# Kernel tuning notes

Hardware: AMD Instinct MI355X
Metric: run time of the kernel (lower is better)

Reference implementation:

```python
import jax, jax.numpy as jnp
import numpy as np

B, C, N, S, DCONV = 16, 128, 2000, 8, 4
DI = 2 * N            # mamba expand=2
DT_RANK = (N + 15) // 16


def setup_inputs() -> dict:
    key = jax.random.key(0)
    ks = jax.random.split(key, 10)
    r = lambda k, sh, s=0.02: jax.random.normal(k, sh, jnp.float32) * s
    return {
        "x": jax.random.normal(ks[0], (B, C, N, 1), jnp.float32),
        "bn1_g": jnp.ones((C,), jnp.float32), "bn1_b": jnp.zeros((C,), jnp.float32),
        "conv1_w": r(ks[1], (C, C)), "conv1_b": jnp.zeros((C,), jnp.float32),
        "ln_w": jnp.ones((N,), jnp.float32), "ln_b": jnp.zeros((N,), jnp.float32),
        "W_in": r(ks[2], (2 * DI, N)),
        "convm_w": r(ks[3], (DI, DCONV), 0.1), "convm_b": jnp.zeros((DI,), jnp.float32),
        "W_x": r(ks[4], (DT_RANK + 2 * S, DI)),
        "W_dt": r(ks[5], (DI, DT_RANK), 0.1), "b_dt": jnp.full((DI,), -2.0, jnp.float32),
        "A_log": jnp.log(jnp.broadcast_to(jnp.arange(1, S + 1, dtype=jnp.float32), (DI, S))),
        "D_p": jnp.ones((DI,), jnp.float32),
        "W_out": r(ks[6], (N, DI)),
        "bn3_g": jnp.ones((C,), jnp.float32), "bn3_b": jnp.zeros((C,), jnp.float32),
        "conv3_w": r(ks[7], (C, C)), "conv3_b": jnp.zeros((C,), jnp.float32),
    }


def _inorm(x, eps=1e-3):
    # InstanceNorm2d (no affine): per-sample, per-channel over spatial dims
    m = x.mean(axis=(2, 3), keepdims=True)
    v = x.var(axis=(2, 3), keepdims=True)
    return (x - m) * jax.lax.rsqrt(v + eps)


def _bnorm(x, g, b, eps=1e-5):
    # BatchNorm2d (training-mode stats) over (B, H, W) per channel
    m = x.mean(axis=(0, 2, 3), keepdims=True)
    v = x.var(axis=(0, 2, 3), keepdims=True)
    return (x - m) * jax.lax.rsqrt(v + eps) * g[None, :, None, None] + b[None, :, None, None]


def _block(x, g, b, w, cb):
    # InstanceNorm -> BatchNorm -> ReLU -> 1x1 Conv2d
    h = jax.nn.relu(_bnorm(_inorm(x), g, b))
    return jnp.einsum('bcnw,oc->bonw', h, w) + cb[None, :, None, None]


def _mamba(u, W_in, cw, cb, W_x, W_dt, b_dt, A_log, D_p, W_out):
    # u: [B, L, D] with L=C (seq), D=N (d_model)
    L = u.shape[1]
    xz = jnp.einsum('bld,ed->ble', u, W_in)          # [B,L,2*DI]
    xi, z = jnp.split(xz, 2, axis=-1)
    # depthwise causal conv1d along L (d_conv=4)
    xp = jnp.pad(xi, ((0, 0), (DCONV - 1, 0), (0, 0)))
    xc = sum(xp[:, k:k + L, :] * cw[:, k] for k in range(DCONV)) + cb
    xc = jax.nn.silu(xc)                             # [B,L,DI]
    xdbl = jnp.einsum('bld,ed->ble', xc, W_x)        # [B,L,dt_rank+2S]
    dt = jax.nn.softplus(jnp.einsum('blr,dr->bld', xdbl[..., :DT_RANK], W_dt) + b_dt)
    Bm = xdbl[..., DT_RANK:DT_RANK + S]              # [B,L,S]
    Cm = xdbl[..., DT_RANK + S:]                     # [B,L,S]
    A = -jnp.exp(A_log)                              # [DI,S]

    def step(h, inp):
        dt_l, B_l, C_l, u_l = inp                    # [B,DI],[B,S],[B,S],[B,DI]
        dA = jnp.exp(dt_l[..., None] * A)            # [B,DI,S]
        h = dA * h + (dt_l * u_l)[..., None] * B_l[:, None, :]
        return h, jnp.einsum('bds,bs->bd', h, C_l)

    seq = (jnp.swapaxes(dt, 0, 1), jnp.swapaxes(Bm, 0, 1),
           jnp.swapaxes(Cm, 0, 1), jnp.swapaxes(xc, 0, 1))
    h0 = jnp.zeros((u.shape[0], DI, S), u.dtype)
    _, ys = jax.lax.scan(step, h0, seq)              # ys: [L,B,DI]
    y = jnp.swapaxes(ys, 0, 1) + xc * D_p
    y = y * jax.nn.silu(z)
    return jnp.einsum('ble,de->bld', y, W_out)       # [B,L,D]


def reference(x, bn1_g, bn1_b, conv1_w, conv1_b, ln_w, ln_b, W_in, convm_w,
              convm_b, W_x, W_dt, b_dt, A_log, D_p, W_out, bn3_g, bn3_b,
              conv3_w, conv3_b):
    out = _block(x, bn1_g, bn1_b, conv1_w, conv1_b)[..., 0]   # [B,C,N]
    mu = out.mean(-1, keepdims=True)
    var = out.var(-1, keepdims=True)
    out_n = (out - mu) * jax.lax.rsqrt(var + 1e-5) * ln_w + ln_b  # LayerNorm(points)
    out = out + _mamba(out_n, W_in, convm_w, convm_b, W_x, W_dt, b_dt, A_log, D_p, W_out)
    out = _block(out[..., None], bn3_g, bn3_b, conv3_w, conv3_b)  # [B,C,N,1]
    return out + x
```

## Files before the change

### kernel.cpp

```cpp
#include <hip/hip_runtime.h>
#include <cmath>
#include <cstdint>

#define Bc   16
#define Cc   128
#define Nc   2000
#define Lc   128
#define DIc  4000
#define Sc   8
#define RKc  125
#define E2c  8000
#define EXc  141

#define KP1  2048
#define NP8  8192
#define KT8  32

__device__ __forceinline__ unsigned short f2bf(float f) {
  union { float f; unsigned int u; } v; v.f = f;
  unsigned int r = v.u + 0x7FFFu + ((v.u >> 16) & 1u);
  return (unsigned short)(r >> 16);
}

__global__ void inorm_stats(const float* __restrict__ in,
                            float* __restrict__ mout,
                            float* __restrict__ vout) {
  int bc = blockIdx.x;
  const float* p = in + (long)bc * Nc;
  float s = 0.f, sq = 0.f;
  for (int i = threadIdx.x; i < Nc; i += blockDim.x) {
    float x = p[i]; s += x; sq += x * x;
  }
  #pragma unroll
  for (int o = 32; o > 0; o >>= 1) {
    s  += __shfl_down(s, o, 64);
    sq += __shfl_down(sq, o, 64);
  }
  __shared__ float ss[4], sqq[4];
  int w = threadIdx.x >> 6, lane = threadIdx.x & 63;
  if (lane == 0) { ss[w] = s; sqq[w] = sq; }
  __syncthreads();
  if (threadIdx.x == 0) {
    s  = ss[0] + ss[1] + ss[2] + ss[3];
    sq = sqq[0] + sqq[1] + sqq[2] + sqq[3];
    float mean = s / Nc;
    float var  = sq / Nc - mean * mean;
    mout[bc] = mean; vout[bc] = var;
  }
}

__global__ void compute_h_t(const float* __restrict__ in,
                            const float* __restrict__ m,
                            const float* __restrict__ v,
                            const float* __restrict__ g,
                            const float* __restrict__ bb,
                            unsigned short* __restrict__ hT) {
  int b  = blockIdx.y;
  int n0 = blockIdx.x * 64;
  __shared__ unsigned short tile[64][132];
  __shared__ float bnsc_s[128];
  int t  = threadIdx.x;
  if (t < 128) {
    float s = 0.f;
    #pragma unroll
    for (int bb2 = 0; bb2 < Bc; bb2++) {
      float vv = v[bb2 * Cc + t];
      s += vv / (vv + 1e-3f);
    }
    bnsc_s[t] = rsqrtf(s / Bc + 1e-5f);
  }
  __syncthreads();
  int nl = t & 63, cb = t >> 6;
  int n  = n0 + nl;
  #pragma unroll 4
  for (int p = 0; p < 32; p++) {
    int c = p * 4 + cb;
    float val = 0.f;
    if (n < Nc) {
      int bc = b * Cc + c;
      float xn = (in[(long)bc * Nc + n] - m[bc]) * rsqrtf(v[bc] + 1e-3f);
      val = fmaxf(xn * bnsc_s[c] * g[c] + bb[c], 0.f);
    }
    tile[nl][c] = f2bf(val);
  }
  __syncthreads();
  int r = t >> 2, c0 = (t & 3) * 32;
  int nr = n0 + r;
  if (nr < Nc) {
    unsigned int* dst = (unsigned int*)(hT + ((long)b * 2048 + nr) * 128 + c0);
    const unsigned short* src = &tile[r][c0];
    #pragma unroll
    for (int j = 0; j < 16; j++)
      dst[j] = *(const unsigned int*)(src + 2 * j);
  }
}

__global__ void reduce_slices(const float* __restrict__ sl, float* __restrict__ dst,
                              long stride, int ns, int total, int accum) {
  int i = blockIdx.x * 256 + threadIdx.x;
  if (i >= total) return;
  float s = accum ? dst[i] : 0.f;
  for (int k = 0; k < ns; k++) s += sl[(long)k * stride + i];
  dst[i] = s;
}

__global__ void reduce_xdbl(const float* __restrict__ sl,
                            float* __restrict__ xd,
                            unsigned short* __restrict__ xdb) {
  int i = blockIdx.x * 256 + threadIdx.x;
  if (i >= 2048 * 144) return;
  int row = i / 144, c = i - row * 144;
  float s = 0.f;
  if (c < EXc) {
    #pragma unroll
    for (int k = 0; k < 4; k++) s += sl[(long)k * (2048 * 256) + (long)row * 256 + c];
    xd[(long)row * EXc + c] = s;
  }
  if (c < 128) xdb[(long)row * 128 + c] = f2bf(c < RKc ? s : 0.f);
}

__global__ void cvt_pad_bf16(const float* __restrict__ src, unsigned short* __restrict__ dst,
                             int R, int Cdst, int Rsrc, int Csrc) {
  long i = (long)blockIdx.x * 256 + threadIdx.x;
  long total = (long)R * Cdst;
  if (i >= total) return;
  int r = (int)(i / Cdst), c = (int)(i - (long)r * Cdst);
  float v = (r < Rsrc && c < Csrc) ? src[(long)r * Csrc + c] : 0.f;
  dst[i] = f2bf(v);
}

__global__ void cvt_convw2(const float* __restrict__ w1, const float* __restrict__ w3,
                           unsigned short* __restrict__ d1, unsigned short* __restrict__ d3) {
  int i = blockIdx.x * 256 + threadIdx.x;
  if (i < 16384) d1[i] = f2bf(w1[i]);
  else if (i < 32768) d3[i - 16384] = f2bf(w3[i - 16384]);
}

__global__ void cvt_wx_wdt(const float* __restrict__ Wx, const float* __restrict__ Wdt,
                           unsigned short* __restrict__ bwx, unsigned short* __restrict__ bwdt) {
  int i = blockIdx.x * 256 + threadIdx.x;
  if (i < 256 * 4000) {
    int r = i / 4000, c = i - r * 4000;
    bwx[i] = f2bf(r < EXc ? Wx[(long)r * 4000 + c] : 0.f);
  } else {
    int j = i - 256 * 4000;
    if (j < 4096 * 128) {
      int r = j >> 7, c = j & 127;
      bwdt[j] = f2bf((r < DIc && c < RKc) ? Wdt[(long)r * RKc + c] : 0.f);
    }
  }
}

__global__ void ln_rows(const float* __restrict__ in,
                        const float* __restrict__ lw,
                        const float* __restrict__ lb,
                        unsigned short* __restrict__ An) {
  int row = blockIdx.x;
  const float* p = in + (long)row * Nc;
  float s = 0.f, sq = 0.f;
  for (int i = threadIdx.x; i < Nc; i += blockDim.x) {
    float x = p[i]; s += x; sq += x * x;
  }
  #pragma unroll
  for (int o = 32; o > 0; o >>= 1) {
    s  += __shfl_down(s, o, 64);
    sq += __shfl_down(sq, o, 64);
  }
  __shared__ float ss[4], sqq[4];
  __shared__ float smean, srstd;
  int w = threadIdx.x >> 6, lane = threadIdx.x & 63;
  if (lane == 0) { ss[w] = s; sqq[w] = sq; }
  __syncthreads();
  if (threadIdx.x == 0) {
    s  = ss[0] + ss[1] + ss[2] + ss[3];
    sq = sqq[0] + sqq[1] + sqq[2] + sqq[3];
    float mean = s / Nc;
    float var  = sq / Nc - mean * mean;
    smean = mean; srstd = rsqrtf(var + 1e-5f);
  }
  __syncthreads();
  float mu = smean, rs = srstd;
  for (int i = threadIdx.x; i < KP1; i += blockDim.x) {
    float v = 0.f;
    if (i < Nc) v = (p[i] - mu) * rs * lw[i] + lb[i];
    An[(long)row * KP1 + i] = f2bf(v);
  }
}

typedef short v8s __attribute__((ext_vector_type(8)));
typedef float v4f __attribute__((ext_vector_type(4)));

typedef const __attribute__((address_space(1))) unsigned int* as1_cu32p;
typedef __attribute__((address_space(3))) unsigned int* as3_u32p;

__device__ __forceinline__ void gload_lds16(const unsigned short* g, unsigned short* l) {
  __builtin_amdgcn_global_load_lds((as1_cu32p)(uintptr_t)g,
                                   (as3_u32p)(uintptr_t)l, 16, 0, 0);
}

__device__ __forceinline__ float gemm_epilogue_val(float v, int epi, int gi, int gj,
                                                   const float* __restrict__ ebias,
                                                   const float* __restrict__ X, long idx) {
  if (epi == 1) {
    float tr = v + ebias[gj];
    float e = __expf(-fabsf(tr));
    v = fmaxf(tr, 0.f) + __logf(1.f + e);
  } else if (epi == 2) {
    if (gj >= DIc) v = v / (1.f + __expf(-v));
  } else if (epi == 3) {
    v += ebias[gi];
    if (X) v += X[idx];
  }
  return v;
}

__global__ __launch_bounds__(256, 4)
void gemm_mfma_bt(const unsigned short* __restrict__ A,
                  const unsigned short* __restrict__ B,
                  float* C, int NN, int K, int lda, int ldb, int ldc,
                  long sA, long sB, long sC,
                  int KS, int Klen, long sliceStride,
                  int epi, const float* __restrict__ ebias,
                  const float* __restrict__ addp) {
  __shared__ unsigned short As[128 * 32];
  __shared__ unsigned short Bs[128 * 32];

  int z = blockIdx.z;
  int batch = z / KS, ks = z - batch * KS;
  const unsigned short* Ab = A + (long)batch * sA;
  const unsigned short* Bb = B + (long)batch * sB;
  float* Cs = C + (long)batch * sC + (long)ks * sliceStride;
  const float* X = addp ? addp + (long)batch * sC : nullptr;

  int k0 = ks * Klen;
  int kend = min(K, k0 + Klen);

  int i0 = blockIdx.y * 128;
  int j0 = blockIdx.x * 128;

  int t = threadIdx.x;
  int wave = t >> 6, lane = t & 63;
  int wm = wave >> 1, wn = wave & 1;

  int srow = lane >> 2;
  int scol = lane & 3;
  const unsigned short* gA0 = Ab + (long)(i0 + wave * 32 + srow) * lda + scol * 8;
  const unsigned short* gA1 = gA0 + (long)16 * lda;
  const unsigned short* gB0 = Bb + (long)(j0 + wave * 32 + srow) * ldb + scol * 8;
  const unsigned short* gB1 = gB0 + (long)16 * ldb;
  unsigned short* lA0 = As + (wave * 32) * 32;
  unsigned short* lA1 = As + (wave * 32 + 16) * 32;
  unsigned short* lB0 = Bs + (wave * 32) * 32;
  unsigned short* lB1 = Bs + (wave * 32 + 16) * 32;

  int fr = lane & 15;
  int kq = lane >> 4;

  v4f acc[4][4] = {};

  for (int kt = k0; kt < kend; kt += 32) {
    gload_lds16(gA0 + kt, lA0);
    gload_lds16(gA1 + kt, lA1);
    gload_lds16(gB0 + kt, lB0);
    gload_lds16(gB1 + kt, lB1);
    __syncthreads();

    v8s af[4], bfr[4];
    #pragma unroll
    for (int mt = 0; mt < 4; mt++)
      af[mt] = *(const v8s*)&As[(wm * 64 + mt * 16 + fr) * 32 + kq * 8];
    #pragma unroll
    for (int nt = 0; nt < 4; nt++)
      bfr[nt] = *(const v8s*)&Bs[(wn * 64 + nt * 16 + fr) * 32 + kq * 8];

    #pragma unroll
    for (int mt = 0; mt < 4; mt++)
      #pragma unroll
      for (int nt = 0; nt < 4; nt++)
        acc[mt][nt] = __builtin_amdgcn_mfma_f32_16x16x32_bf16(
            af[mt], bfr[nt], acc[mt][nt], 0, 0, 0);
    __syncthreads();
  }

  int orow = (lane >> 4) * 4;
  int ocol = lane & 15;
  #pragma unroll
  for (int mt = 0; mt < 4; mt++) {
    #pragma unroll
    for (int nt = 0; nt < 4; nt++) {
      int gi = i0 + wm * 64 + mt * 16 + orow;
      int gj = j0 + wn * 64 + nt * 16 + ocol;
      if (gj >= NN) continue;
      #pragma unroll
      for (int r = 0; r < 4; r++) {
        long idx = (long)(gi + r) * ldc + gj;
        Cs[idx] = gemm_epilogue_val(acc[mt][nt][r], epi, gi + r, gj, ebias, X, idx);
      }
    }
  }
}

__global__ __launch_bounds__(256, 2)
void gemm_k128(const unsigned short* __restrict__ A,
               const unsigned short* __restrict__ B,
               float* C, int NN, int ldc,
               long sA, long sB, long sC,
               int epi, const float* __restrict__ ebias,
               const float* __restrict__ addp) {
  __shared__ unsigned short As[4 * 128 * 32];
  __shared__ unsigned short Bs[4 * 128 * 32];

  int batch = blockIdx.z;
  const unsigned short* Ab = A + (long)batch * sA;
  const unsigned short* Bb = B + (long)batch * sB;
  float* Cs = C + (long)batch * sC;
  const float* X = addp ? addp + (long)batch * sC : nullptr;

  int i0 = blockIdx.y * 128;
  int j0 = blockIdx.x * 128;

  int t = threadIdx.x;
  int wave = t >> 6, lane = t & 63;
  int wm = wave >> 1, wn = wave & 1;
  int srow = lane >> 2, scol = lane & 3;

  const unsigned short* gA0 = Ab + (long)(i0 + wave * 32 + srow) * 128 + scol * 8;
  const unsigned short* gB0 = Bb + (long)(j0 + wave * 32 + srow) * 128 + scol * 8;

  #pragma unroll
  for (int kt = 0; kt < 4; kt++) {
    gload_lds16(gA0 + kt * 32,            As + kt * 4096 + (wave * 32) * 32);
    gload_lds16(gA0 + 16 * 128 + kt * 32, As + kt * 4096 + (wave * 32 + 16) * 32);
    gload_lds16(gB0 + kt * 32,            Bs + kt * 4096 + (wave * 32) * 32);
    gload_lds16(gB0 + 16 * 128 + kt * 32, Bs + kt * 4096 + (wave * 32 + 16) * 32);
  }
  __syncthreads();

  int fr = lane & 15, kq = lane >> 4;
  v4f acc[4][4] = {};
  #pragma unroll
  for (int kk = 0; kk < 4; kk++) {
    v8s af[4], bfr[4];
    #pragma unroll
    for (int mt = 0; mt < 4; mt++)
      af[mt] = *(const v8s*)&As[kk * 4096 + (wm * 64 + mt * 16 + fr) * 32 + kq * 8];
    #pragma unroll
    for (int nt = 0; nt < 4; nt++)
      bfr[nt] = *(const v8s*)&Bs[kk * 4096 + (wn * 64 + nt * 16 + fr) * 32 + kq * 8];
    #pragma unroll
    for (int mt = 0; mt < 4; mt++)
      #pragma unroll
      for (int nt = 0; nt < 4; nt++)
        acc[mt][nt] = __builtin_amdgcn_mfma_f32_16x16x32_bf16(
            af[mt], bfr[nt], acc[mt][nt], 0, 0, 0);
  }

  int orow = (lane >> 4) * 4;
  int ocol = lane & 15;
  #pragma unroll
  for (int mt = 0; mt < 4; mt++) {
    #pragma unroll
    for (int nt = 0; nt < 4; nt++) {
      int gi = i0 + wm * 64 + mt * 16 + orow;
      int gj = j0 + wn * 64 + nt * 16 + ocol;
      if (gj >= NN) continue;
      #pragma unroll
      for (int r = 0; r < 4; r++) {
        long idx = (long)(gi + r) * ldc + gj;
        Cs[idx] = gemm_epilogue_val(acc[mt][nt][r], epi, gi + r, gj, ebias, X, idx);
      }
    }
  }
}

#define MM(mh, nh) do {                                                       \
    _Pragma("unroll")                                                         \
    for (int mt_ = 0; mt_ < 4; mt_++) {                                       \
      _Pragma("unroll")                                                       \
      for (int nt_ = 0; nt_ < 2; nt_++) {                                     \
        acc[(mh) * 4 + mt_][(nh) * 2 + nt_] = __builtin_amdgcn_mfma_f32_16x16x32_bf16( \
            aF[mt_][0], bF[nh][nt_][0], acc[(mh) * 4 + mt_][(nh) * 2 + nt_], 0, 0, 0); \
        acc[(mh) * 4 + mt_][(nh) * 2 + nt_] = __builtin_amdgcn_mfma_f32_16x16x32_bf16( \
            aF[mt_][1], bF[nh][nt_][1], acc[(mh) * 4 + mt_][(nh) * 2 + nt_], 0, 0, 0); \
      } }                                                                     \
  } while (0)
#define FENCE()   __asm__ volatile("" ::: "memory")
#define BARRIER() do { FENCE(); __builtin_amdgcn_s_barrier(); FENCE(); } while (0)
#define WAIT_LGKM0() do { __asm__ volatile("s_waitcnt lgkmcnt(0)" ::: "memory"); \
                          __builtin_amdgcn_sched_barrier(0); } while (0)
#define WAIT_VM(n) __asm__ volatile("s_waitcnt vmcnt(" #n ")" ::: "memory")

__global__ __launch_bounds__(512, 2)
void gemm_win_8ph(const unsigned short* __restrict__ A,
                  const unsigned short* __restrict__ B,
                  float* __restrict__ C) {
  __shared__ unsigned short As8[2 * 2 * 128 * 64];
  __shared__ unsigned short Bs8[2 * 2 * 128 * 64];

  const int lda = KP1, ldb = KP1, ldc = E2c;

  int i0 = blockIdx.y * 256;
  int j0 = blockIdx.x * 256;

  int t = threadIdx.x;
  int w = t >> 6, l = t & 63;
  int wm = w >> 2;
  int wn = w & 3;
  int w8 = w << 3;

  int rw     = w8 + (l >> 3);
  int scol16 = (l & 7) ^ ((l >> 3) & 7);
  const unsigned short* pA = A + (long)(i0 + rw) * lda + scol16 * 8;
  int gjrow = ((rw >> 5) << 6) + (rw & 31);
  const unsigned short* pB = B + (long)(j0 + gjrow) * ldb + scol16 * 8;

  int fr   = l & 15;
  int kq   = l >> 4;
  int inr0 = ((kq ^ (fr & 7)) << 4);
  int inr1 = inr0 ^ 64;

  const char* asb = (const char*)As8;
  const char* bsb = (const char*)Bs8;

  v4f acc[8][4] = {};
  v8s aF[4][2], bF[2][2][2];

#define ST_A(bufi, h, tile) do {                                              \
    int kt_ = ((tile) < KT8 ? (tile) : (KT8 - 1)) * 64;                       \
    gload_lds16(pA + (long)((h) * 64) * lda + kt_,                            \
                As8 + (size_t)((((bufi) * 2 + (h)) * 128 + w8) * 64));        \
    gload_lds16(pA + (long)(128 + (h) * 64) * lda + kt_,                      \
                As8 + (size_t)((((bufi) * 2 + (h)) * 128 + 64 + w8) * 64));   \
  } while (0)
#define ST_B(bufi, h, tile) do {                                              \
    int kt_ = ((tile) < KT8 ? (tile) : (KT8 - 1)) * 64;                       \
    gload_lds16(pB + (long)((h) * 32) * ldb + kt_,                            \
                Bs8 + (size_t)((((bufi) * 2 + (h)) * 128 + w8) * 64));        \
    gload_lds16(pB + (long)(128 + (h) * 32) * ldb + kt_,                      \
                Bs8 + (size_t)((((bufi) * 2 + (h)) * 128 + 64 + w8) * 64));   \
  } while (0)
#define LD_A(bufi, mh) do {                                                   \
    const char* ab_ = asb + (size_t)(((((bufi) * 2 + (mh)) * 128) + wm * 64 + fr) * 128); \
    aF[0][0] = *(const v8s*)(ab_ +    0 + inr0); aF[0][1] = *(const v8s*)(ab_ +    0 + inr1); \
    aF[1][0] = *(const v8s*)(ab_ + 2048 + inr0); aF[1][1] = *(const v8s*)(ab_ + 2048 + inr1); \
    aF[2][0] = *(const v8s*)(ab_ + 4096 + inr0); aF[2][1] = *(const v8s*)(ab_ + 4096 + inr1); \
    aF[3][0] = *(const v8s*)(ab_ + 6144 + inr0); aF[3][1] = *(const v8s*)(ab_ + 6144 + inr1); \
  } while (0)
#define LD_B(bufi, nh) do {                                                   \
    const char* bb_ = bsb + (size_t)(((((bufi) * 2 + (nh)) * 128) + wn * 32 + fr) * 128); \
    bF[nh][0][0] = *(const v8s*)(bb_ +    0 + inr0); bF[nh][0][1] = *(const v8s*)(bb_ +    0 + inr1); \
    bF[nh][1][0] = *(const v8s*)(bb_ + 2048 + inr0); bF[nh][1][1] = *(const v8s*)(bb_ + 2048 + inr1); \
  } while (0)

  ST_A(0, 0, 0); ST_B(0, 0, 0); ST_B(0, 1, 0); ST_A(0, 1, 0);
  ST_A(1, 0, 1); ST_B(1, 1, 1); ST_A(1, 1, 1);
  WAIT_VM(6);
  BARRIER();

  #pragma unroll 1
  for (int it = 0; it < KT8 / 2; ++it) {
    int u = 2 * it;
    LD_A(0, 0); LD_B(0, 0); ST_B(1, 0, u + 1);
    BARRIER(); WAIT_LGKM0();
    __builtin_amdgcn_s_setprio(1); MM(0, 0); __builtin_amdgcn_s_setprio(0);
    BARRIER();
    LD_B(0, 1); ST_A(0, 0, u + 2);
    BARRIER(); WAIT_LGKM0();
    __builtin_amdgcn_s_setprio(1); MM(0, 1); __builtin_amdgcn_s_setprio(0);
    BARRIER();
    LD_A(0, 1); ST_B(0, 1, u + 2);
    BARRIER(); WAIT_LGKM0();
    __builtin_amdgcn_s_setprio(1); MM(1, 1); __builtin_amdgcn_s_setprio(0);
    BARRIER();
    ST_A(0, 1, u + 2);
    BARRIER();
    __builtin_amdgcn_s_setprio(1); MM(1, 0); __builtin_amdgcn_s_setprio(0);
    WAIT_VM(6);
    BARRIER();
    LD_A(1, 0); LD_B(1, 0); ST_B(0, 0, u + 2);
    BARRIER(); WAIT_LGKM0();
    __builtin_amdgcn_s_setprio(1); MM(0, 0); __builtin_amdgcn_s_setprio(0);
    BARRIER();
    LD_B(1, 1); ST_A(1, 0, u + 3);
    BARRIER(); WAIT_LGKM0();
    __builtin_amdgcn_s_setprio(1); MM(0, 1); __builtin_amdgcn_s_setprio(0);
    BARRIER();
    LD_A(1, 1); ST_B(1, 1, u + 3);
    BARRIER(); WAIT_LGKM0();
    __builtin_amdgcn_s_setprio(1); MM(1, 1); __builtin_amdgcn_s_setprio(0);
    BARRIER();
    ST_A(1, 1, u + 3);
    BARRIER();
    __builtin_amdgcn_s_setprio(1); MM(1, 0); __builtin_amdgcn_s_setprio(0);
    WAIT_VM(6);
    BARRIER();
  }
  WAIT_VM(0);

  int orow4 = (l >> 4) * 4;
  int ocol  = l & 15;
  #pragma unroll
  for (int m = 0; m < 8; m++) {
    int gi = i0 + wm * 128 + m * 16 + orow4;
    #pragma unroll
    for (int n = 0; n < 4; n++) {
      int gj = j0 + wn * 64 + n * 16 + ocol;
      if (gj >= E2c) continue;
      #pragma unroll
      for (int r = 0; r < 4; r++) {
        float v = acc[m][n][r];
        if (gj >= DIc) v = v / (1.f + __expf(-v));
        C[(long)(gi + r) * ldc + gj] = v;
      }
    }
  }
#undef ST_A
#undef ST_B
#undef LD_A
#undef LD_B
}

__global__ __launch_bounds__(512, 2)
void gemm_wout_8ph(const unsigned short* __restrict__ A,
                   const unsigned short* __restrict__ B,
                   float* __restrict__ C,
                   const unsigned short* __restrict__ zsrc) {
  __shared__ unsigned short As8[2 * 2 * 128 * 64];
  __shared__ unsigned short Bs8[2 * 2 * 128 * 64];

  const int lda = 4000, ldb = 4000;

  int i0 = blockIdx.y * 256;
  int j0 = blockIdx.x * 256;
  int ks = blockIdx.z;
  int k0t = ks * 16;

  int t = threadIdx.x;
  int w = t >> 6, l = t & 63;
  int wm = w >> 2;
  int wn = w & 3;
  int w8 = w << 3;

  int rw     = w8 + (l >> 3);
  int scol16 = (l & 7) ^ ((l >> 3) & 7);
  const unsigned short* pA = A + (long)(i0 + rw) * lda + scol16 * 8;
  int gjrow = ((rw >> 5) << 6) + (rw & 31);
  const unsigned short* pB = B + (long)(j0 + gjrow) * ldb + scol16 * 8;

  int fr   = l & 15;
  int kq   = l >> 4;
  int inr0 = ((kq ^ (fr & 7)) << 4);
  int inr1 = inr0 ^ 64;

  const char* asb = (const char*)As8;
  const char* bsb = (const char*)Bs8;

  v4f acc[8][4] = {};
  v8s aF[4][2], bF[2][2][2];

#define ST_A2(bufi, h, lt) do {                                               \
    int gk_ = k0t + (((lt) < 16) ? (lt) : 15);                                \
    bool pad_ = (gk_ >= 62) && (gk_ == 63 || scol16 >= 4);                    \
    const unsigned short* s0_ = pad_ ? zsrc : pA + (long)((h) * 64) * lda + gk_ * 64;   \
    const unsigned short* s1_ = pad_ ? zsrc : pA + (long)(128 + (h) * 64) * lda + gk_ * 64; \
    gload_lds16(s0_, As8 + (size_t)((((bufi) * 2 + (h)) * 128 + w8) * 64));   \
    gload_lds16(s1_, As8 + (size_t)((((bufi) * 2 + (h)) * 128 + 64 + w8) * 64)); \
  } while (0)
#define ST_B2(bufi, h, lt) do {                                               \
    int gk_ = k0t + (((lt) < 16) ? (lt) : 15);                                \
    bool pad_ = (gk_ >= 62) && (gk_ == 63 || scol16 >= 4);                    \
    const unsigned short* s0_ = pad_ ? zsrc : pB + (long)((h) * 32) * ldb + gk_ * 64;   \
    const unsigned short* s1_ = pad_ ? zsrc : pB + (long)(128 + (h) * 32) * ldb + gk_ * 64; \
    gload_lds16(s0_, Bs8 + (size_t)((((bufi) * 2 + (h)) * 128 + w8) * 64));   \
    gload_lds16(s1_, Bs8 + (size_t)((((bufi) * 2 + (h)) * 128 + 64 + w8) * 64)); \
  } while (0)
#define LD_A2(bufi, mh) do {                                                  \
    const char* ab_ = asb + (size_t)(((((bufi) * 2 + (mh)) * 128) + wm * 64 + fr) * 128); \
    aF[0][0] = *(const v8s*)(ab_ +    0 + inr0); aF[0][1] = *(const v8s*)(ab_ +    0 + inr1); \
    aF[1][0] = *(const v8s*)(ab_ + 2048 + inr0); aF[1][1] = *(const v8s*)(ab_ + 2048 + inr1); \
    aF[2][0] = *(const v8s*)(ab_ + 4096 + inr0); aF[2][1] = *(const v8s*)(ab_ + 4096 + inr1); \
    aF[3][0] = *(const v8s*)(ab_ + 6144 + inr0); aF[3][1] = *(const v8s*)(ab_ + 6144 + inr1); \
  } while (0)
#define LD_B2(bufi, nh) do {                                                  \
    const char* bb_ = bsb + (size_t)(((((bufi) * 2 + (nh)) * 128) + wn * 32 + fr) * 128); \
    bF[nh][0][0] = *(const v8s*)(bb_ +    0 + inr0); bF[nh][0][1] = *(const v8s*)(bb_ +    0 + inr1); \
    bF[nh][1][0] = *(const v8s*)(bb_ + 2048 + inr0); bF[nh][1][1] = *(const v8s*)(bb_ + 2048 + inr1); \
  } while (0)

  ST_A2(0, 0, 0); ST_B2(0, 0, 0); ST_B2(0, 1, 0); ST_A2(0, 1, 0);
  ST_A2(1, 0, 1); ST_B2(1, 1, 1); ST_A2(1, 1, 1);
  WAIT_VM(6);
  BARRIER();

  #pragma unroll 1
  for (int it = 0; it < 8; ++it) {
    int u = 2 * it;
    LD_A2(0, 0); LD_B2(0, 0); ST_B2(1, 0, u + 1);
    BARRIER(); WAIT_LGKM0();
    __builtin_amdgcn_s_setprio(1); MM(0, 0); __builtin_amdgcn_s_setprio(0);
    BARRIER();
    LD_B2(0, 1); ST_A2(0, 0, u + 2);
    BARRIER(); WAIT_LGKM0();
    __builtin_amdgcn_s_setprio(1); MM(0, 1); __builtin_amdgcn_s_setprio(0);
    BARRIER();
    LD_A2(0, 1); ST_B2(0, 1, u + 2);
    BARRIER(); WAIT_LGKM0();
    __builtin_amdgcn_s_setprio(1); MM(1, 1); __builtin_amdgcn_s_setprio(0);
    BARRIER();
    ST_A2(0, 1, u + 2);
    BARRIER();
    __builtin_amdgcn_s_setprio(1); MM(1, 0); __builtin_amdgcn_s_setprio(0);
    WAIT_VM(6);
    BARRIER();
    LD_A2(1, 0); LD_B2(1, 0); ST_B2(0, 0, u + 2);
    BARRIER(); WAIT_LGKM0();
    __builtin_amdgcn_s_setprio(1); MM(0, 0); __builtin_amdgcn_s_setprio(0);
    BARRIER();
    LD_B2(1, 1); ST_A2(1, 0, u + 3);
    BARRIER(); WAIT_LGKM0();
    __builtin_amdgcn_s_setprio(1); MM(0, 1); __builtin_amdgcn_s_setprio(0);
    BARRIER();
    LD_A2(1, 1); ST_B2(1, 1, u + 3);
    BARRIER(); WAIT_LGKM0();
    __builtin_amdgcn_s_setprio(1); MM(1, 1); __builtin_amdgcn_s_setprio(0);
    BARRIER();
    ST_A2(1, 1, u + 3);
    BARRIER();
    __builtin_amdgcn_s_setprio(1); MM(1, 0); __builtin_amdgcn_s_setprio(0);
    WAIT_VM(6);
    BARRIER();
  }
  WAIT_VM(0);

  float* Cs = C + (long)ks * ((long)2048 * Nc);
  int orow4 = (l >> 4) * 4;
  int ocol  = l & 15;
  #pragma unroll
  for (int m = 0; m < 8; m++) {
    int gi = i0 + wm * 128 + m * 16 + orow4;
    #pragma unroll
    for (int n = 0; n < 4; n++) {
      int gj = j0 + wn * 64 + n * 16 + ocol;
      if (gj >= Nc) continue;
      #pragma unroll
      for (int r = 0; r < 4; r++)
        Cs[(long)(gi + r) * Nc + gj] = acc[m][n][r];
    }
  }
#undef ST_A2
#undef ST_B2
#undef LD_A2
#undef LD_B2
}

#undef MM
#undef FENCE
#undef BARRIER
#undef WAIT_LGKM0
#undef WAIT_VM

__global__ void dwconv_silu(const float* __restrict__ xz,
                            const float4* __restrict__ cw,
                            const float* __restrict__ cb,
                            float* __restrict__ xc,
                            unsigned short* __restrict__ xcb, int total) {
  int i = blockIdx.x * 256 + threadIdx.x;
  if (i >= total) return;
  int d  = i % DIc;
  int bl = i / DIc;
  int l  = bl % Lc;
  int b  = bl / Lc;
  float4 w = cw[d];
  float acc = cb[d];
  long rowbase = (long)(b * Lc) * E2c + d;
  int l0 = l - 3;
  if (l0     >= 0) acc += xz[rowbase + (long)l0       * E2c] * w.x;
  if (l0 + 1 >= 0) acc += xz[rowbase + (long)(l0 + 1) * E2c] * w.y;
  if (l0 + 2 >= 0) acc += xz[rowbase + (long)(l0 + 2) * E2c] * w.z;
  acc += xz[rowbase + (long)l * E2c] * w.w;
  float sv = acc / (1.f + __expf(-acc));
  xc[i] = sv;
  xcb[i] = f2bf(sv);
}

#define SCU 4
__global__ __launch_bounds__(256)
void scan_kernel(const float* __restrict__ dtv,
                 const float* __restrict__ xdbl,
                 const float* __restrict__ xc,
                 const float* __restrict__ xzf,
                 const float* __restrict__ A_log,
                 const float* __restrict__ D_p,
                 unsigned short* __restrict__ yb) {
  int d = blockIdx.x * 256 + threadIdx.x;
  int b = blockIdx.y;
  if (d >= DIc) return;
  float Av[Sc];
  #pragma unroll
  for (int s = 0; s < Sc; s++) Av[s] = -__expf(A_log[d * Sc + s]);
  float Dp = D_p[d];
  float h[Sc];
  #pragma unroll
  for (int s = 0; s < Sc; s++) h[s] = 0.f;

  long base  = (long)(b * Lc) * DIc + d;
  long zbase = (long)(b * Lc) * E2c + DIc + d;
  const float* xrow = xdbl + (long)(b * Lc) * EXc + RKc;

  float d0[SCU], u0[SCU], z0[SCU], B0[SCU][Sc], C0[SCU][Sc];
  float d1[SCU], u1[SCU], z1[SCU], B1[SCU][Sc], C1[SCU][Sc];

#define LOADG(g, dd, uu, zz, BB, CC)                                        \
  { int l0_ = (g) * SCU;                                                    \
    _Pragma("unroll")                                                       \
    for (int u = 0; u < SCU; u++) {                                         \
      long idx = base + (long)(l0_ + u) * DIc;                              \
      dd[u] = dtv[idx];                                                     \
      uu[u] = xc[idx];                                                      \
      zz[u] = xzf[zbase + (long)(l0_ + u) * E2c];                           \
      const float* xr = xrow + (long)(l0_ + u) * EXc;                       \
      _Pragma("unroll")                                                     \
      for (int s = 0; s < Sc; s++) { BB[u][s] = xr[s]; CC[u][s] = xr[Sc + s]; } \
    } }

#define COMPG(g, dd, uu, zz, BB, CC)                                        \
  { int l0_ = (g) * SCU;                                                    \
    _Pragma("unroll")                                                       \
    for (int u = 0; u < SCU; u++) {                                         \
      float dv = dd[u], uv = uu[u];                                         \
      float du = dv * uv;                                                   \
      float p = 0.f;                                                        \
      _Pragma("unroll")                                                     \
      for (int s = 0; s < Sc; s++) {                                        \
        float dA = __expf(dv * Av[s]);                                      \
        h[s] = dA * h[s] + du * BB[u][s];                                   \
        p += h[s] * CC[u][s];                                               \
      }                                                                     \
      yb[base + (long)(l0_ + u) * DIc] = f2bf((p + uv * Dp) * zz[u]);       \
    } }

  LOADG(0, d0, u0, z0, B0, C0);
  #pragma unroll 1
  for (int g = 0; g < Lc / SCU; g += 2) {
    LOADG(g + 1, d1, u1, z1, B1, C1);
    COMPG(g, d0, u0, z0, B0, C0);
    if (g + 2 < Lc / SCU) LOADG(g + 2, d0, u0, z0, B0, C0);
    COMPG(g + 1, d1, u1, z1, B1, C1);
  }
#undef LOADG
#undef COMPG
}

extern "C" void kernel_launch(void* const* d_in, const int* in_sizes, int n_in,
                              void* d_out, int out_size, void* d_ws, size_t ws_size,
                              hipStream_t stream) {
  const float* x       = (const float*)d_in[0];
  const float* bn1_g   = (const float*)d_in[1];
  const float* bn1_b   = (const float*)d_in[2];
  const float* conv1_w = (const float*)d_in[3];
  const float* conv1_b = (const float*)d_in[4];
  const float* ln_w    = (const float*)d_in[5];
  const float* ln_b    = (const float*)d_in[6];
  const float* W_in    = (const float*)d_in[7];
  const float* convm_w = (const float*)d_in[8];
  const float* convm_b = (const float*)d_in[9];
  const float* W_x     = (const float*)d_in[10];
  const float* W_dt    = (const float*)d_in[11];
  const float* b_dt    = (const float*)d_in[12];
  const float* A_log   = (const float*)d_in[13];
  const float* D_p     = (const float*)d_in[14];
  const float* W_out   = (const float*)d_in[15];
  const float* bn3_g   = (const float*)d_in[16];
  const float* bn3_b   = (const float*)d_in[17];
  const float* conv3_w = (const float*)d_in[18];
  const float* conv3_b = (const float*)d_in[19];
  float* out = (float*)d_out;
  float* ws  = (float*)d_ws;

  const int TOT  = Bc * Cc * Nc;
  const int ROWS = Bc * Lc;

  float* m1    = ws;
  float* v1    = ws + 2048;
  float* h     = ws + 8192;
  float* out1  = h    + (long)TOT;
  float* outn  = out1 + (long)TOT;
  float* xz    = outn + (long)TOT;
  float* xc    = xz   + (long)ROWS * E2c;
  float* xdbl  = xc   + (long)ROWS * DIc;
  float* dtb   = xdbl + (long)ROWS * EXc;

  unsigned short* An      = (unsigned short*)outn;
  unsigned short* Bwin8   = (unsigned short*)xc;
  unsigned short* Bwx     = (unsigned short*)outn;
  unsigned short* Bwdt    = (unsigned short*)(outn + 512000);
  float*          xdbl_sl = outn + 800000;
  unsigned short* xdbl_b  = (unsigned short*)(outn + 2900000);
  unsigned short* W1b     = (unsigned short*)(outn + 3100000);
  unsigned short* W3b     = (unsigned short*)(outn + 3200000);
  unsigned short* hT      = (unsigned short*)h;
  unsigned short* xcb     = (unsigned short*)h;
  unsigned short* Bwout   = (unsigned short*)h;
  unsigned short* yb      = (unsigned short*)out;
  float*          wout_sl = xz;
  const unsigned short* zsrc = (const unsigned short*)(outn + 768000);

  dim3 b256(256);
  int gElem = (TOT + 255) / 256;

  cvt_convw2<<<dim3(128), b256, 0, stream>>>(conv1_w, conv3_w, W1b, W3b);

  inorm_stats<<<dim3(Bc * Cc), b256, 0, stream>>>(x, m1, v1);
  compute_h_t<<<dim3(32, Bc), b256, 0, stream>>>(x, m1, v1, bn1_g, bn1_b, hT);
  {
    dim3 g(16, 1, Bc);
    gemm_k128<<<g, b256, 0, stream>>>(W1b, hT, out1, Nc, Nc,
                                      0L, 2048L * 128, (long)Cc * Nc,
                                      3, conv1_b, nullptr);
  }

  ln_rows<<<dim3(ROWS), b256, 0, stream>>>(out1, ln_w, ln_b, An);

  {
    long tot = (long)NP8 * KP1;
    cvt_pad_bf16<<<dim3((unsigned)((tot + 255) / 256)), b256, 0, stream>>>(
        W_in, Bwin8, NP8, KP1, E2c, Nc);
  }

  gemm_win_8ph<<<dim3(NP8 / 256, ROWS / 256), dim3(512), 0, stream>>>(An, Bwin8, xz);

  cvt_wx_wdt<<<dim3((256 * 4000 + 4096 * 128 + 255) / 256), b256, 0, stream>>>(
      W_x, W_dt, Bwx, Bwdt);

  {
    int tot = ROWS * DIc;
    dwconv_silu<<<dim3((tot + 255) / 256), b256, 0, stream>>>(
        xz, (const float4*)convm_w, convm_b, xc, xcb, tot);
  }

  {
    dim3 g(2, ROWS / 128, 4);
    gemm_mfma_bt<<<g, b256, 0, stream>>>(xcb, Bwx, xdbl_sl, 256, DIc,
                                         DIc, DIc, 256, 0L, 0L, 0L,
                                         4, 1024, 2048L * 256, 0, nullptr, nullptr);
    int tot = 2048 * 144;
    reduce_xdbl<<<dim3((tot + 255) / 256), b256, 0, stream>>>(xdbl_sl, xdbl, xdbl_b);
  }

  {
    dim3 g(4096 / 128, ROWS / 128, 1);
    gemm_k128<<<g, b256, 0, stream>>>(xdbl_b, Bwdt, dtb, DIc, DIc,
                                      0L, 0L, 0L, 1, b_dt, nullptr);
  }

  {
    long tot = (long)2048 * DIc;
    cvt_pad_bf16<<<dim3((unsigned)((tot + 255) / 256)), b256, 0, stream>>>(
        W_out, Bwout, 2048, DIc, Nc, DIc);
  }

  scan_kernel<<<dim3((DIc + 255) / 256, Bc), b256, 0, stream>>>(
      dtb, xdbl, xc, xz, A_log, D_p, yb);

  gemm_wout_8ph<<<dim3(8, 8, 4), dim3(512), 0, stream>>>(yb, Bwout, wout_sl, zsrc);
  reduce_slices<<<dim3(gElem), b256, 0, stream>>>(
      wout_sl, out1, (long)TOT, 4, TOT, 1);

  inorm_stats<<<dim3(Bc * Cc), b256, 0, stream>>>(out1, m1, v1);
  compute_h_t<<<dim3(32, Bc), b256, 0, stream>>>(out1, m1, v1, bn3_g, bn3_b, hT);
  {
    dim3 g(16, 1, Bc);
    gemm_k128<<<g, b256, 0, stream>>>(W3b, hT, out, Nc, Nc,
                                      0L, 2048L * 128, (long)Cc * Nc,
                                      3, conv3_b, x);
  }
}
```

Baseline: 579.2 us.

## Fuse split-K reduction with instance-norm stats and vectorize conversion kernels

```diff
diff --git a/kernel.cpp b/kernel.cpp
--- a/kernel.cpp
+++ b/kernel.cpp
@@ -11,6 +11,7 @@
 #define RKc  125
 #define E2c  8000
 #define EXc  141
+#define TOTc (Bc * Cc * Nc)
 
 #define KP1  2048
 #define NP8  8192
@@ -30,6 +31,37 @@
   float s = 0.f, sq = 0.f;
   for (int i = threadIdx.x; i < Nc; i += blockDim.x) {
     float x = p[i]; s += x; sq += x * x;
+  }
+  #pragma unroll
+  for (int o = 32; o > 0; o >>= 1) {
+    s  += __shfl_down(s, o, 64);
+    sq += __shfl_down(sq, o, 64);
+  }
+  __shared__ float ss[4], sqq[4];
+  int w = threadIdx.x >> 6, lane = threadIdx.x & 63;
+  if (lane == 0) { ss[w] = s; sqq[w] = sq; }
+  __syncthreads();
+  if (threadIdx.x == 0) {
+    s  = ss[0] + ss[1] + ss[2] + ss[3];
+    sq = sqq[0] + sqq[1] + sqq[2] + sqq[3];
+    float mean = s / Nc;
+    float var  = sq / Nc - mean * mean;
+    mout[bc] = mean; vout[bc] = var;
+  }
+}
+
+__global__ void reduce_stats(const float* __restrict__ sl,
+                             float* __restrict__ dst,
+                             float* __restrict__ mout,
+                             float* __restrict__ vout) {
+  int bc = blockIdx.x;
+  long base = (long)bc * Nc;
+  float s = 0.f, sq = 0.f;
+  for (int n = threadIdx.x; n < Nc; n += blockDim.x) {
+    long i = base + n;
+    float v = dst[i] + sl[i] + sl[i + (long)TOTc] + sl[i + 2L * TOTc] + sl[i + 3L * TOTc];
+    dst[i] = v;
+    s += v; sq += v * v;
   }
   #pragma unroll
   for (int o = 32; o > 0; o >>= 1) {
@@ -95,15 +127,6 @@
   }
 }
 
-__global__ void reduce_slices(const float* __restrict__ sl, float* __restrict__ dst,
-                              long stride, int ns, int total, int accum) {
-  int i = blockIdx.x * 256 + threadIdx.x;
-  if (i >= total) return;
-  float s = accum ? dst[i] : 0.f;
-  for (int k = 0; k < ns; k++) s += sl[(long)k * stride + i];
-  dst[i] = s;
-}
-
 __global__ void reduce_xdbl(const float* __restrict__ sl,
                             float* __restrict__ xd,
                             unsigned short* __restrict__ xdb) {
@@ -113,20 +136,37 @@
   float s = 0.f;
   if (c < EXc) {
     #pragma unroll
-    for (int k = 0; k < 4; k++) s += sl[(long)k * (2048 * 256) + (long)row * 256 + c];
+    for (int k = 0; k < 8; k++) s += sl[(long)k * (2048 * 256) + (long)row * 256 + c];
     xd[(long)row * EXc + c] = s;
   }
   if (c < 128) xdb[(long)row * 128 + c] = f2bf(c < RKc ? s : 0.f);
 }
 
-__global__ void cvt_pad_bf16(const float* __restrict__ src, unsigned short* __restrict__ dst,
-                             int R, int Cdst, int Rsrc, int Csrc) {
-  long i = (long)blockIdx.x * 256 + threadIdx.x;
-  long total = (long)R * Cdst;
-  if (i >= total) return;
-  int r = (int)(i / Cdst), c = (int)(i - (long)r * Cdst);
-  float v = (r < Rsrc && c < Csrc) ? src[(long)r * Csrc + c] : 0.f;
-  dst[i] = f2bf(v);
+__global__ void cvt_win_v4(const float* __restrict__ W, unsigned short* __restrict__ dst) {
+  int i = blockIdx.x * 256 + threadIdx.x;
+  int r  = i >> 9;
+  int c4 = (i & 511) << 2;
+  uint2 o = make_uint2(0u, 0u);
+  if (r < E2c && c4 < Nc) {
+    float4 v = *(const float4*)&W[(long)r * Nc + c4];
+    o.x = (unsigned)f2bf(v.x) | ((unsigned)f2bf(v.y) << 16);
+    o.y = (unsigned)f2bf(v.z) | ((unsigned)f2bf(v.w) << 16);
+  }
+  *(uint2*)&dst[(long)r * KP1 + c4] = o;
+}
+
+__global__ void cvt_wout_v4(const float* __restrict__ W, unsigned short* __restrict__ dst) {
+  int i = blockIdx.x * 256 + threadIdx.x;
+  if (i >= 2048 * 1000) return;
+  int r  = i / 1000;
+  int c4 = (i - r * 1000) << 2;
+  uint2 o = make_uint2(0u, 0u);
+  if (r < Nc) {
+    float4 v = *(const float4*)&W[(long)r * DIc + c4];
+    o.x = (unsigned)f2bf(v.x) | ((unsigned)f2bf(v.y) << 16);
+    o.y = (unsigned)f2bf(v.z) | ((unsigned)f2bf(v.w) << 16);
+  }
+  *(uint2*)&dst[(long)r * DIc + c4] = o;
 }
 
 __global__ void cvt_convw2(const float* __restrict__ w1, const float* __restrict__ w3,
@@ -659,28 +699,35 @@
 #undef WAIT_LGKM0
 #undef WAIT_VM
 
-__global__ void dwconv_silu(const float* __restrict__ xz,
-                            const float4* __restrict__ cw,
-                            const float* __restrict__ cb,
-                            float* __restrict__ xc,
-                            unsigned short* __restrict__ xcb, int total) {
+__global__ void dwconv_silu2(const float* __restrict__ xz,
+                             const float4* __restrict__ cw,
+                             const float* __restrict__ cb,
+                             float* __restrict__ xc,
+                             unsigned short* __restrict__ xcb, int totalPairs) {
   int i = blockIdx.x * 256 + threadIdx.x;
-  if (i >= total) return;
-  int d  = i % DIc;
-  int bl = i / DIc;
+  if (i >= totalPairs) return;
+  int p  = i % (DIc / 2);
+  int bl = i / (DIc / 2);
+  int d  = p * 2;
   int l  = bl % Lc;
   int b  = bl / Lc;
-  float4 w = cw[d];
-  float acc = cb[d];
+  float4 w0 = cw[d], w1 = cw[d + 1];
+  float a0 = cb[d], a1 = cb[d + 1];
   long rowbase = (long)(b * Lc) * E2c + d;
   int l0 = l - 3;
-  if (l0     >= 0) acc += xz[rowbase + (long)l0       * E2c] * w.x;
-  if (l0 + 1 >= 0) acc += xz[rowbase + (long)(l0 + 1) * E2c] * w.y;
-  if (l0 + 2 >= 0) acc += xz[rowbase + (long)(l0 + 2) * E2c] * w.z;
-  acc += xz[rowbase + (long)l * E2c] * w.w;
-  float sv = acc / (1.f + __expf(-acc));
-  xc[i] = sv;
-  xcb[i] = f2bf(sv);
+  if (l0 >= 0)     { float2 v = *(const float2*)&xz[rowbase + (long)l0 * E2c];
+                     a0 += v.x * w0.x; a1 += v.y * w1.x; }
+  if (l0 + 1 >= 0) { float2 v = *(const float2*)&xz[rowbase + (long)(l0 + 1) * E2c];
+                     a0 += v.x * w0.y; a1 += v.y * w1.y; }
+  if (l0 + 2 >= 0) { float2 v = *(const float2*)&xz[rowbase + (long)(l0 + 2) * E2c];
+                     a0 += v.x * w0.z; a1 += v.y * w1.z; }
+  { float2 v = *(const float2*)&xz[rowbase + (long)l * E2c];
+    a0 += v.x * w0.w; a1 += v.y * w1.w; }
+  float s0 = a0 / (1.f + __expf(-a0));
+  float s1 = a1 / (1.f + __expf(-a1));
+  long o = (long)bl * DIc + d;
+  *(float2*)&xc[o] = make_float2(s0, s1);
+  *(unsigned int*)&xcb[o] = (unsigned)f2bf(s0) | ((unsigned)f2bf(s1) << 16);
 }
 
 #define SCU 4
@@ -777,7 +824,7 @@
   float* out = (float*)d_out;
   float* ws  = (float*)d_ws;
 
-  const int TOT  = Bc * Cc * Nc;
+  const int TOT  = TOTc;
   const int ROWS = Bc * Lc;
 
   float* m1    = ws;
@@ -794,7 +841,7 @@
   unsigned short* Bwin8   = (unsigned short*)xc;
   unsigned short* Bwx     = (unsigned short*)outn;
   unsigned short* Bwdt    = (unsigned short*)(outn + 512000);
-  float*          xdbl_sl = outn + 800000;
+  float*          xdbl_sl = dtb;
   unsigned short* xdbl_b  = (unsigned short*)(outn + 2900000);
   unsigned short* W1b     = (unsigned short*)(outn + 3100000);
   unsigned short* W3b     = (unsigned short*)(outn + 3200000);
@@ -806,7 +853,6 @@
   const unsigned short* zsrc = (const unsigned short*)(outn + 768000);
 
   dim3 b256(256);
-  int gElem = (TOT + 255) / 256;
 
   cvt_convw2<<<dim3(128), b256, 0, stream>>>(conv1_w, conv3_w, W1b, W3b);
 
@@ -821,11 +867,7 @@
 
   ln_rows<<<dim3(ROWS), b256, 0, stream>>>(out1, ln_w, ln_b, An);
 
-  {
-    long tot = (long)NP8 * KP1;
-    cvt_pad_bf16<<<dim3((unsigned)((tot + 255) / 256)), b256, 0, stream>>>(
-        W_in, Bwin8, NP8, KP1, E2c, Nc);
-  }
+  cvt_win_v4<<<dim3(NP8 * 512 / 256), b256, 0, stream>>>(W_in, Bwin8);
 
   gemm_win_8ph<<<dim3(NP8 / 256, ROWS / 256), dim3(512), 0, stream>>>(An, Bwin8, xz);
 
@@ -833,16 +875,16 @@
       W_x, W_dt, Bwx, Bwdt);
 
   {
-    int tot = ROWS * DIc;
-    dwconv_silu<<<dim3((tot + 255) / 256), b256, 0, stream>>>(
-        xz, (const float4*)convm_w, convm_b, xc, xcb, tot);
+    int totalPairs = ROWS * DIc / 2;
+    dwconv_silu2<<<dim3((totalPairs + 255) / 256), b256, 0, stream>>>(
+        xz, (const float4*)convm_w, convm_b, xc, xcb, totalPairs);
   }
 
   {
-    dim3 g(2, ROWS / 128, 4);
+    dim3 g(2, ROWS / 128, 8);
     gemm_mfma_bt<<<g, b256, 0, stream>>>(xcb, Bwx, xdbl_sl, 256, DIc,
                                          DIc, DIc, 256, 0L, 0L, 0L,
-                                         4, 1024, 2048L * 256, 0, nullptr, nullptr);
+                                         8, 512, 2048L * 256, 0, nullptr, nullptr);
     int tot = 2048 * 144;
     reduce_xdbl<<<dim3((tot + 255) / 256), b256, 0, stream>>>(xdbl_sl, xdbl, xdbl_b);
   }
@@ -853,20 +895,15 @@
                                       0L, 0L, 0L, 1, b_dt, nullptr);
   }
 
-  {
-    long tot = (long)2048 * DIc;
-    cvt_pad_bf16<<<dim3((unsigned)((tot + 255) / 256)), b256, 0, stream>>>(
-        W_out, Bwout, 2048, DIc, Nc, DIc);
-  }
+  cvt_wout_v4<<<dim3((2048 * 1000 + 255) / 256), b256, 0, stream>>>(W_out, Bwout);
 
   scan_kernel<<<dim3((DIc + 255) / 256, Bc), b256, 0, stream>>>(
       dtb, xdbl, xc, xz, A_log, D_p, yb);
 
   gemm_wout_8ph<<<dim3(8, 8, 4), dim3(512), 0, stream>>>(yb, Bwout, wout_sl, zsrc);
-  reduce_slices<<<dim3(gElem), b256, 0, stream>>>(
-      wout_sl, out1, (long)TOT, 4, TOT, 1);
-
-  inorm_stats<<<dim3(Bc * Cc), b256, 0, stream>>>(out1, m1, v1);
+
+  reduce_stats<<<dim3(Bc * Cc), b256, 0, stream>>>(wout_sl, out1, m1, v1);
+
   compute_h_t<<<dim3(32, Bc), b256, 0, stream>>>(out1, m1, v1, bn3_g, bn3_b, hT);
   {
     dim3 g(16, 1, Bc);
```

New measurement: 535.7 us (median of 2 runs). -7.5%, faster.
